# Kernel optimization log

Hardware: AMD Instinct MI355X
Metric: run time of the kernel (lower is better)

The kernel has to match this reference:

```python
import jax, jax.numpy as jnp
import numpy as np

B, T, TEMP, H, M = 2048, 168, 128, 1024, 48


def lstm_cell(x, h, c, Wih, Whh, bih, bhh):
    # PyTorch gate order: i, f, g, o
    gates = x @ Wih.T + h @ Whh.T + bih + bhh  # [B, 4H]
    i, f, g, o = jnp.split(gates, 4, axis=-1)
    i = jax.nn.sigmoid(i)
    f = jax.nn.sigmoid(f)
    g = jnp.tanh(g)
    o = jax.nn.sigmoid(o)
    c_new = f * c + i * g
    h_new = o * jnp.tanh(c_new)
    return h_new, c_new


def setup_inputs() -> dict:
    key = jax.random.key(0)
    ks = jax.random.split(key, 12)
    s_e = 1.0 / np.sqrt(H)
    u = lambda k, shape: jax.random.uniform(k, shape, jnp.float32, -s_e, s_e)
    return {
        "temp_seq": jax.random.normal(ks[0], (B, T, TEMP), jnp.float32),
        "avg_speeds": jax.random.normal(ks[1], (B, M), jnp.float32),
        "enc_Wih": u(ks[2], (4 * H, TEMP)),
        "enc_Whh": u(ks[3], (4 * H, H)),
        "enc_bih": u(ks[4], (4 * H,)),
        "enc_bhh": u(ks[5], (4 * H,)),
        "dec_Wih": u(ks[6], (4 * H, TEMP + 1)),
        "dec_Whh": u(ks[7], (4 * H, H)),
        "dec_bih": u(ks[8], (4 * H,)),
        "dec_bhh": u(ks[9], (4 * H,)),
        "fc_W": u(ks[10], (TEMP, H)),
        "fc_b": u(ks[11], (TEMP,)),
    }


def reference(temp_seq, avg_speeds, enc_Wih, enc_Whh, enc_bih, enc_bhh,
              dec_Wih, dec_Whh, dec_bih, dec_bhh, fc_W, fc_b):
    b = temp_seq.shape[0]
    h0 = jnp.zeros((b, H), temp_seq.dtype)
    c0 = jnp.zeros((b, H), temp_seq.dtype)

    # Encoder: LSTM over time, keep only final (h, c)
    def enc_step(carry, x_t):
        h, c = carry
        h, c = lstm_cell(x_t, h, c, enc_Wih, enc_Whh, enc_bih, enc_bhh)
        return (h, c), None

    (h_n, c_n), _ = jax.lax.scan(enc_step, (h0, c0), jnp.swapaxes(temp_seq, 0, 1))

    input_temp0 = temp_seq[:, -1, :]  # [B, TEMP]

    def dec_step(carry, speed_t):
        h, c, x_temp = carry
        x = jnp.concatenate([x_temp, speed_t[:, None]], axis=-1)  # [B, TEMP+1]
        h, c = lstm_cell(x, h, c, dec_Wih, dec_Whh, dec_bih, dec_bhh)
        pred = h @ fc_W.T + fc_b  # [B, TEMP]
        return (h, c, pred), pred

    _, preds = jax.lax.scan(dec_step, (h_n, c_n, input_temp0),
                            jnp.swapaxes(avg_speeds, 0, 1))
    return jnp.swapaxes(preds, 0, 1)  # [B, M, TEMP]
```

## Files before the change

### kernel.cpp

```cpp
#include <hip/hip_runtime.h>
#include <stdint.h>

#define B_SZ   2048
#define T_ENC  168
#define TEMPD  128
#define HID    1024
#define M_DEC  48

typedef _Float16 f16;
typedef _Float16 half8 __attribute__((ext_vector_type(8)));
typedef float    f32x4 __attribute__((ext_vector_type(4)));

__device__ __forceinline__ float sigf(float x)   { return 1.0f / (1.0f + __expf(-x)); }
__device__ __forceinline__ float tanhf_(float x) { return 2.0f / (1.0f + __expf(-2.0f * x)) - 1.0f; }

__device__ __forceinline__ void gld16(const void* g, void* l) {
    __builtin_amdgcn_global_load_lds(
        (const __attribute__((address_space(1))) void*)g,
        (__attribute__((address_space(3))) void*)l, 16, 0, 0);
}

__global__ void prep_xseq(const float* __restrict__ temp_seq, f16* __restrict__ xseq)
{
    size_t i4 = ((size_t)blockIdx.x * blockDim.x + threadIdx.x) * 4;
    size_t b  = i4 / (T_ENC * TEMPD);
    size_t r  = i4 - b * (T_ENC * TEMPD);
    size_t t  = r >> 7;
    size_t d  = r & 127;
    float4 v = *(const float4*)(temp_seq + i4);
    f16* o = xseq + ((t * B_SZ) + b) * TEMPD + d;
    o[0] = (f16)v.x; o[1] = (f16)v.y; o[2] = (f16)v.z; o[3] = (f16)v.w;
}

__global__ void prep_misc(
    const float* __restrict__ encWih, const float* __restrict__ encWhh,
    const float* __restrict__ decWih, const float* __restrict__ decWhh,
    const float* __restrict__ encbih, const float* __restrict__ encbhh,
    const float* __restrict__ decbih, const float* __restrict__ decbhh,
    const float* __restrict__ fcW,
    f16* __restrict__ Wenc, f16* __restrict__ Wdec0, f16* __restrict__ fcWh,
    float* __restrict__ enc_b, float* __restrict__ dec_b, float* __restrict__ wlast)
{
    const int NW = 4 * HID * (TEMPD + HID);
    for (int idx = blockIdx.x * blockDim.x + threadIdx.x; idx < NW;
         idx += gridDim.x * blockDim.x) {
        int j = idx / (TEMPD + HID);
        int k = idx - j * (TEMPD + HID);
        Wenc[idx]  = (f16)(k < TEMPD ? encWih[j * TEMPD + k]
                                     : encWhh[(size_t)j * HID + (k - TEMPD)]);
        Wdec0[idx] = (f16)(k < TEMPD ? decWih[j * (TEMPD + 1) + k]
                                     : decWhh[(size_t)j * HID + (k - TEMPD)]);
        if (idx < TEMPD * HID) fcWh[idx] = (f16)fcW[idx];
        if (idx < 4 * HID) {
            enc_b[idx] = encbih[idx] + encbhh[idx];
            dec_b[idx] = decbih[idx] + decbhh[idx];
            wlast[idx] = decWih[idx * (TEMPD + 1) + TEMPD];
        }
    }
}

__global__ __launch_bounds__(256)
void prep_fold(
    const float* __restrict__ decWih, const float* __restrict__ decWhh,
    const float* __restrict__ decbih, const float* __restrict__ decbhh,
    const float* __restrict__ fcW,    const float* __restrict__ fcb,
    f16* __restrict__ WdecF, float* __restrict__ biasF)
{
    __shared__ float wih[16][TEMPD];
    __shared__ float fcbL[TEMPD];
    const int tid = threadIdx.x;
    const int j0  = blockIdx.x * 16;
    for (int i = tid; i < 16 * TEMPD; i += 256) {
        int r = i >> 7, p = i & 127;
        wih[r][p] = decWih[(size_t)(j0 + r) * (TEMPD + 1) + p];
    }
    if (tid < TEMPD) fcbL[tid] = fcb[tid];
    __syncthreads();
    for (int kk = 0; kk < 4; ++kk) {
        int k = kk * 256 + tid;
        float acc[16];
        #pragma unroll
        for (int r = 0; r < 16; ++r) acc[r] = decWhh[(size_t)(j0 + r) * HID + k];
        for (int p = 0; p < TEMPD; ++p) {
            float w = fcW[(size_t)p * HID + k];
            #pragma unroll
            for (int r = 0; r < 16; ++r) acc[r] += wih[r][p] * w;
        }
        #pragma unroll
        for (int r = 0; r < 16; ++r) WdecF[(size_t)(j0 + r) * HID + k] = (f16)acc[r];
    }
    if (tid < 16) {
        float b = decbih[j0 + tid] + decbhh[j0 + tid];
        for (int p = 0; p < TEMPD; ++p) b += wih[tid][p] * fcbL[p];
        biasF[j0 + tid] = b;
    }
}

__global__ void prep_tileW(const f16* __restrict__ Wsrc, f16* __restrict__ Wt,
                           int NKC, int WS)
{
    int idx = blockIdx.x * blockDim.x + threadIdx.x;
    int total = 32 * NKC * 16 * 64;
    if (idx >= total) return;
    int lane = idx & 63;
    int f    = idx >> 6;
    int wc   = f & 1;
    int g    = (f >> 1) & 3;
    int s    = (f >> 3) & 1;
    int kc   = (f >> 4) % NKC;
    int bn   = (f >> 4) / NKC;
    int row  = g * HID + bn * 32 + wc * 16 + (lane & 15);
    int k0   = kc * 64 + s * 32 + (lane >> 4) * 8;
    *(half8*)(Wt + (size_t)idx * 8) = *(const half8*)(Wsrc + (size_t)row * WS + k0);
}

template <int FULLK, int DEC>
__global__ __launch_bounds__(256, 2)
void lstm_step(
    const f16* __restrict__ xsrc,
    const f16* __restrict__ h_in, f16* __restrict__ h_out, float* __restrict__ c,
    const f16* __restrict__ Wt,
    const float* __restrict__ bias,
    const float* __restrict__ wlast, const float* __restrict__ speeds, int m_step)
{
    constexpr int NKC = FULLK ? 18 : 16;

    __shared__ half8 ldsA[2][1024];

    const int tid  = threadIdx.x;
    const int lane = tid & 63;
    const int wid  = tid >> 6;
    const int wr   = wid >> 1;
    const int wc   = wid & 1;
    const int id   = blockIdx.x;
    const int swzb = (id & 7) * 64 + (id >> 3);
    const int bn   = swzb >> 4;
    const int bm   = swzb & 15;

    const half8* wtb = (const half8*)Wt + ((size_t)bn * NKC * 16) * 64 + wc * 64 + lane;

    f32x4 acc[4][4];
    #pragma unroll
    for (int g = 0; g < 4; ++g)
        #pragma unroll
        for (int mr = 0; mr < 4; ++mr)
            acc[g][mr] = (f32x4){0.f, 0.f, 0.f, 0.f};

    auto stageA = [&](int b, int kc) {
        if (FULLK && kc < 2) {
            #pragma unroll
            for (int it = 0; it < 4; ++it) {
                int p = wid * 256 + it * 64 + lane;
                int row = p >> 3, s = p & 7;
                gld16(xsrc + (size_t)(bm * 128 + row) * TEMPD + kc * 64 + ((s ^ (row & 7)) << 3),
                      &ldsA[b][wid * 256 + it * 64]);
            }
        } else {
            const int k0 = kc * 64 - (FULLK ? TEMPD : 0);
            #pragma unroll
            for (int it = 0; it < 4; ++it) {
                int p = wid * 256 + it * 64 + lane;
                int row = p >> 3, s = p & 7;
                gld16(h_in + (size_t)(bm * 128 + row) * HID + k0 + ((s ^ (row & 7)) << 3),
                      &ldsA[b][wid * 256 + it * 64]);
            }
        }
    };
    auto loadW = [&](half8 (&wf)[8], int kc) {
        const half8* p = wtb + (size_t)kc * (16 * 64);
        #pragma unroll
        for (int f = 0; f < 8; ++f) wf[f] = p[f * 128];
    };
    auto compute = [&](int b, const half8 (&wf)[8]) {
        #pragma unroll
        for (int s = 0; s < 2; ++s) {
            const int ks = s * 4 + (lane >> 4);
            half8 af[4];
            #pragma unroll
            for (int mr = 0; mr < 4; ++mr) {
                int row = wr * 64 + mr * 16 + (lane & 15);
                af[mr] = ldsA[b][row * 8 + (ks ^ (row & 7))];
            }
            __builtin_amdgcn_s_setprio(1);
            #pragma unroll
            for (int g = 0; g < 4; ++g)
                #pragma unroll
                for (int mr = 0; mr < 4; ++mr)
                    acc[g][mr] = __builtin_amdgcn_mfma_f32_16x16x32_f16(af[mr], wf[s * 4 + g], acc[g][mr], 0, 0, 0);
            __builtin_amdgcn_s_setprio(0);
        }
    };

    half8 wfA[8], wfB[8];
    stageA(0, 0); loadW(wfA, 0);
    __syncthreads();

    for (int kc = 0; kc < NKC; kc += 2) {
        stageA(1, kc + 1); loadW(wfB, kc + 1);
        compute(0, wfA);
        __syncthreads();
        if (kc + 2 < NKC) { stageA(0, kc + 2); loadW(wfA, kc + 2); }
        compute(1, wfB);
        __syncthreads();
    }

    const int col_g = bn * 32 + wc * 16 + (lane & 15);
    const float bi  = bias[col_g];
    const float bf_ = bias[HID + col_g];
    const float bg  = bias[2 * HID + col_g];
    const float bo  = bias[3 * HID + col_g];
    float wli = 0.f, wlf = 0.f, wlg = 0.f, wlo = 0.f;
    if (DEC) {
        wli = wlast[col_g];
        wlf = wlast[HID + col_g];
        wlg = wlast[2 * HID + col_g];
        wlo = wlast[3 * HID + col_g];
    }
    #pragma unroll
    for (int mr = 0; mr < 4; ++mr) {
        #pragma unroll
        for (int q = 0; q < 4; ++q) {
            int row_g = bm * 128 + wr * 64 + mr * 16 + (lane >> 4) * 4 + q;
            float pi = acc[0][mr][q] + bi;
            float pf = acc[1][mr][q] + bf_;
            float pg = acc[2][mr][q] + bg;
            float po = acc[3][mr][q] + bo;
            if (DEC) {
                float sp = speeds[(size_t)row_g * M_DEC + m_step];
                pi += sp * wli; pf += sp * wlf; pg += sp * wlg; po += sp * wlo;
            }
            float ii = sigf(pi), ff = sigf(pf), gg = tanhf_(pg), oo = sigf(po);
            size_t idx = (size_t)row_g * HID + col_g;
            float cn = ff * c[idx] + ii * gg;
            c[idx] = cn;
            h_out[idx] = (f16)(oo * tanhf_(cn));
        }
    }
}

__global__ __launch_bounds__(256, 2)
void fc_batch(const f16* __restrict__ hist, const f16* __restrict__ fcWh,
              const float* __restrict__ fcb, float* __restrict__ out, int mbase)
{
    __shared__ half8 ldsA[32 * 8];
    __shared__ half8 ldsW[128 * 8];
    const int tid  = threadIdx.x;
    const int lane = tid & 63;
    const int wid  = tid >> 6;
    const int wr   = wid >> 1;
    const int wc   = wid & 1;
    const int bm   = blockIdx.x;
    const int slot = bm >> 6;
    const int b0   = (bm & 63) * 32;
    const f16* hrow = hist + (size_t)slot * (B_SZ * HID) + (size_t)b0 * HID;
    const int  mm   = mbase + slot;

    f32x4 acc[4];
    #pragma unroll
    for (int nr = 0; nr < 4; ++nr) acc[nr] = (f32x4){0.f, 0.f, 0.f, 0.f};

    for (int kc = 0; kc < HID / 64; ++kc) {
        const int k0 = kc * 64;
        {
            int row = tid >> 3, s = tid & 7;
            gld16(hrow + (size_t)row * HID + k0 + ((s ^ (row & 7)) << 3), &ldsA[wid * 64]);
        }
        #pragma unroll
        for (int it = 0; it < 4; ++it) {
            int p = wid * 256 + it * 64 + lane;
            int row = p >> 3, s = p & 7;
            gld16(fcWh + (size_t)row * HID + k0 + ((s ^ (row & 7)) << 3), &ldsW[wid * 256 + it * 64]);
        }
        __syncthreads();
        #pragma unroll
        for (int s2 = 0; s2 < 2; ++s2) {
            int arow = wr * 16 + (lane & 15);
            int slotk = s2 * 4 + (lane >> 4);
            half8 a = ldsA[arow * 8 + (slotk ^ (arow & 7))];
            #pragma unroll
            for (int nr = 0; nr < 4; ++nr) {
                int brow = wc * 64 + nr * 16 + (lane & 15);
                half8 bfr = ldsW[brow * 8 + (slotk ^ (brow & 7))];
                acc[nr] = __builtin_amdgcn_mfma_f32_16x16x32_f16(a, bfr, acc[nr], 0, 0, 0);
            }
        }
        __syncthreads();
    }
    #pragma unroll
    for (int nr = 0; nr < 4; ++nr)
        #pragma unroll
        for (int q = 0; q < 4; ++q) {
            int rloc = wr * 16 + (lane >> 4) * 4 + q;
            int col  = wc * 64 + nr * 16 + (lane & 15);
            out[(size_t)(b0 + rloc) * (M_DEC * TEMPD) + (size_t)mm * TEMPD + col] = acc[nr][q] + fcb[col];
        }
}

extern "C" void kernel_launch(void* const* d_in, const int* in_sizes, int n_in,
                              void* d_out, int out_size, void* d_ws, size_t ws_size,
                              hipStream_t stream)
{
    (void)in_sizes; (void)n_in; (void)out_size; (void)ws_size;
    const float* temp_seq   = (const float*)d_in[0];
    const float* avg_speeds = (const float*)d_in[1];
    const float* enc_Wih    = (const float*)d_in[2];
    const float* enc_Whh    = (const float*)d_in[3];
    const float* enc_bih    = (const float*)d_in[4];
    const float* enc_bhh    = (const float*)d_in[5];
    const float* dec_Wih    = (const float*)d_in[6];
    const float* dec_Whh    = (const float*)d_in[7];
    const float* dec_bih    = (const float*)d_in[8];
    const float* dec_bhh    = (const float*)d_in[9];
    const float* fc_W       = (const float*)d_in[10];
    const float* fc_b       = (const float*)d_in[11];
    float* out = (float*)d_out;

    char* ws = (char*)d_ws;
    size_t off = 0;
    auto alloc = [&](size_t bytes) -> void* {
        void* p = ws + off;
        off += (bytes + 255) & ~(size_t)255;
        return p;
    };
    const size_t SLOT = (size_t)B_SZ * HID;
    f16*   Wenc   = (f16*)alloc((size_t)4 * HID * (TEMPD + HID) * 2);
    f16*   Wdec0  = (f16*)alloc((size_t)4 * HID * (TEMPD + HID) * 2);
    f16*   WdecF  = (f16*)alloc((size_t)4 * HID * HID * 2);
    f16*   WencT  = (f16*)alloc((size_t)32 * 18 * 16 * 64 * 8 * 2);
    f16*   Wdec0T = (f16*)alloc((size_t)32 * 18 * 16 * 64 * 8 * 2);
    f16*   WdecFT = (f16*)alloc((size_t)32 * 16 * 16 * 64 * 8 * 2);
    f16*   fcWh   = (f16*)alloc((size_t)TEMPD * HID * 2);
    float* enc_b  = (float*)alloc((size_t)4 * HID * 4);
    float* dec_b  = (float*)alloc((size_t)4 * HID * 4);
    float* biasF  = (float*)alloc((size_t)4 * HID * 4);
    float* wlast  = (float*)alloc((size_t)4 * HID * 4);
    f16*   hA     = (f16*)alloc(SLOT * 2);
    f16*   hB     = (f16*)alloc(SLOT * 2);
    float* cbuf   = (float*)alloc(SLOT * 4);
    f16*   xseq   = (f16*)alloc((size_t)T_ENC * B_SZ * TEMPD * 2);
    f16*   hist   = (f16*)alloc(16 * SLOT * 2);

    hipMemsetAsync(hA,   0, SLOT * 2, stream);
    hipMemsetAsync(cbuf, 0, SLOT * 4, stream);

    prep_xseq<<<(B_SZ * T_ENC * TEMPD / 4 + 255) / 256, 256, 0, stream>>>(temp_seq, xseq);
    prep_misc<<<8192, 256, 0, stream>>>(
        enc_Wih, enc_Whh, dec_Wih, dec_Whh,
        enc_bih, enc_bhh, dec_bih, dec_bhh, fc_W,
        Wenc, Wdec0, fcWh, enc_b, dec_b, wlast);
    prep_fold<<<256, 256, 0, stream>>>(
        dec_Wih, dec_Whh, dec_bih, dec_bhh, fc_W, fc_b, WdecF, biasF);
    prep_tileW<<<(32 * 18 * 16 * 64 + 255) / 256, 256, 0, stream>>>(Wenc,  WencT,  18, TEMPD + HID);
    prep_tileW<<<(32 * 18 * 16 * 64 + 255) / 256, 256, 0, stream>>>(Wdec0, Wdec0T, 18, TEMPD + HID);
    prep_tileW<<<(32 * 16 * 16 * 64 + 255) / 256, 256, 0, stream>>>(WdecF, WdecFT, 16, HID);

    f16* hbuf[2] = {hA, hB};
    for (int t = 0; t < T_ENC; ++t) {
        lstm_step<1, 0><<<512, 256, 0, stream>>>(
            xseq + (size_t)t * (B_SZ * TEMPD),
            hbuf[t & 1], hbuf[(t + 1) & 1], cbuf,
            WencT, enc_b, nullptr, nullptr, 0);
    }
    for (int m = 0; m < M_DEC; ++m) {
        const f16* hin = (m == 0) ? hA : hist + ((size_t)((m - 1) & 15)) * SLOT;
        f16* hout = hist + ((size_t)(m & 15)) * SLOT;
        if (m == 0) {
            lstm_step<1, 1><<<512, 256, 0, stream>>>(
                xseq + (size_t)(T_ENC - 1) * (B_SZ * TEMPD),
                hin, hout, cbuf, Wdec0T, dec_b, wlast, avg_speeds, 0);
        } else {
            lstm_step<0, 1><<<512, 256, 0, stream>>>(
                nullptr, hin, hout, cbuf, WdecFT, biasF, wlast, avg_speeds, m);
        }
        if ((m & 15) == 15) {
            fc_batch<<<1024, 256, 0, stream>>>(hist, fcWh, fc_b, out, m - 15);
        }
    }
}
```

Measured before the change: 6.319 ms.

## Fuse all LSTM steps into one persistent kernel with a software grid barrier

Replaces the 216 per-step kernel launches and the three FC batch launches with a single persistent kernel of 512 blocks. Blocks step through the encoder and decoder timesteps and synchronise with an atomic generation-counter grid barrier between steps. The FC projection over all 48 stored decoder states then runs at the end, so the history buffer grows to 48 slots. This is meant to remove launch and drain gaps between steps, but correctness depends on all 512 blocks being co-resident. The barrier also has a spin timeout that could break synchronisation silently.

New measurement: 18.04 ms. 186% more time.

```diff
diff --git a/kernel.cpp b/kernel.cpp
--- a/kernel.cpp
+++ b/kernel.cpp
@@ -6,6 +6,7 @@
 #define TEMPD  128
 #define HID    1024
 #define M_DEC  48
+#define NBLK   512
 
 typedef _Float16 f16;
 typedef _Float16 half8 __attribute__((ext_vector_type(8)));
@@ -114,19 +115,43 @@
     *(half8*)(Wt + (size_t)idx * 8) = *(const half8*)(Wsrc + (size_t)row * WS + k0);
 }
 
-template <int FULLK, int DEC>
+struct PK {
+    const f16* xseq; f16* hA; f16* hB; float* c;
+    const f16* WencT; const f16* Wdec0T; const f16* WdecFT;
+    const float* enc_b; const float* dec_b; const float* biasF;
+    const float* wlast; const float* speeds;
+    f16* hist; const f16* fcWh; const float* fcb; float* out;
+    unsigned* cnt; unsigned* gen;
+};
+
+__device__ __forceinline__ void gridbar(unsigned* cnt, unsigned* gen)
+{
+    __syncthreads();
+    if (threadIdx.x == 0) {
+        unsigned g = __hip_atomic_load(gen, __ATOMIC_RELAXED, __HIP_MEMORY_SCOPE_AGENT);
+        __builtin_amdgcn_fence(__ATOMIC_RELEASE, "agent");
+        unsigned a = __hip_atomic_fetch_add(cnt, 1u, __ATOMIC_RELAXED, __HIP_MEMORY_SCOPE_AGENT);
+        if (a == NBLK - 1) {
+            __hip_atomic_store(cnt, 0u, __ATOMIC_RELAXED, __HIP_MEMORY_SCOPE_AGENT);
+            __hip_atomic_store(gen, g + 1u, __ATOMIC_RELEASE, __HIP_MEMORY_SCOPE_AGENT);
+        } else {
+            long spin = 0;
+            while (__hip_atomic_load(gen, __ATOMIC_RELAXED, __HIP_MEMORY_SCOPE_AGENT) == g) {
+                __builtin_amdgcn_s_sleep(1);
+                if (++spin > 400000) break;
+            }
+        }
+        __builtin_amdgcn_fence(__ATOMIC_ACQUIRE, "agent");
+    }
+    __syncthreads();
+}
+
 __global__ __launch_bounds__(256, 2)
-void lstm_step(
-    const f16* __restrict__ xsrc,
-    const f16* __restrict__ h_in, f16* __restrict__ h_out, float* __restrict__ c,
-    const f16* __restrict__ Wt,
-    const float* __restrict__ bias,
-    const float* __restrict__ wlast, const float* __restrict__ speeds, int m_step)
-{
-    constexpr int NKC = FULLK ? 18 : 16;
-
-    __shared__ half8 ldsA[2][1024];
-
+void persist(PK p)
+{
+    __shared__ half8 smem[2048];
+
+    const size_t SLOT = (size_t)B_SZ * HID;
     const int tid  = threadIdx.x;
     const int lane = tid & 63;
     const int wid  = tid >> 6;
@@ -137,163 +162,176 @@
     const int bn   = swzb >> 4;
     const int bm   = swzb & 15;
 
-    const half8* wtb = (const half8*)Wt + ((size_t)bn * NKC * 16) * 64 + wc * 64 + lane;
-
-    f32x4 acc[4][4];
-    #pragma unroll
-    for (int g = 0; g < 4; ++g)
-        #pragma unroll
-        for (int mr = 0; mr < 4; ++mr)
-            acc[g][mr] = (f32x4){0.f, 0.f, 0.f, 0.f};
-
-    auto stageA = [&](int b, int kc) {
-        if (FULLK && kc < 2) {
+    for (int step = 0; step < T_ENC + M_DEC; ++step) {
+        const int m = step - T_ENC;
+        const f16* Wt; const float* bias; const f16* xsrc;
+        const f16* hin; f16* hout;
+        int nkc, fullk, dec;
+        if (step < T_ENC) {
+            Wt = p.WencT; bias = p.enc_b; nkc = 18; fullk = 1; dec = 0;
+            xsrc = p.xseq + (size_t)step * (B_SZ * TEMPD);
+            hin  = (step & 1) ? p.hB : p.hA;
+            hout = (step & 1) ? p.hA : p.hB;
+        } else if (m == 0) {
+            Wt = p.Wdec0T; bias = p.dec_b; nkc = 18; fullk = 1; dec = 1;
+            xsrc = p.xseq + (size_t)(T_ENC - 1) * (B_SZ * TEMPD);
+            hin  = p.hA;
+            hout = p.hist;
+        } else {
+            Wt = p.WdecFT; bias = p.biasF; nkc = 16; fullk = 0; dec = 1;
+            xsrc = nullptr;
+            hin  = p.hist + (size_t)(m - 1) * SLOT;
+            hout = p.hist + (size_t)m * SLOT;
+        }
+        const half8* wtb = (const half8*)Wt + (size_t)bn * nkc * 16 * 64 + wc * 64 + lane;
+
+        f32x4 acc[4][4];
+        #pragma unroll
+        for (int g = 0; g < 4; ++g)
+            #pragma unroll
+            for (int mr = 0; mr < 4; ++mr)
+                acc[g][mr] = (f32x4){0.f, 0.f, 0.f, 0.f};
+
+        auto stageA = [&](int b, int kc) {
+            if (fullk && kc < 2) {
+                #pragma unroll
+                for (int it = 0; it < 4; ++it) {
+                    int pc = wid * 256 + it * 64 + lane;
+                    int row = pc >> 3, s = pc & 7;
+                    gld16(xsrc + (size_t)(bm * 128 + row) * TEMPD + kc * 64 + ((s ^ (row & 7)) << 3),
+                          &smem[b * 1024 + wid * 256 + it * 64]);
+                }
+            } else {
+                const int k0 = kc * 64 - (fullk ? TEMPD : 0);
+                #pragma unroll
+                for (int it = 0; it < 4; ++it) {
+                    int pc = wid * 256 + it * 64 + lane;
+                    int row = pc >> 3, s = pc & 7;
+                    gld16(hin + (size_t)(bm * 128 + row) * HID + k0 + ((s ^ (row & 7)) << 3),
+                          &smem[b * 1024 + wid * 256 + it * 64]);
+                }
+            }
+        };
+        auto loadW = [&](half8 (&wf)[8], int kc) {
+            const half8* pw = wtb + (size_t)kc * (16 * 64);
+            #pragma unroll
+            for (int f = 0; f < 8; ++f) wf[f] = pw[f * 128];
+        };
+        auto compute = [&](int b, const half8 (&wf)[8]) {
+            #pragma unroll
+            for (int s = 0; s < 2; ++s) {
+                const int ks = s * 4 + (lane >> 4);
+                half8 af[4];
+                #pragma unroll
+                for (int mr = 0; mr < 4; ++mr) {
+                    int row = wr * 64 + mr * 16 + (lane & 15);
+                    af[mr] = smem[b * 1024 + row * 8 + (ks ^ (row & 7))];
+                }
+                __builtin_amdgcn_s_setprio(1);
+                #pragma unroll
+                for (int g = 0; g < 4; ++g)
+                    #pragma unroll
+                    for (int mr = 0; mr < 4; ++mr)
+                        acc[g][mr] = __builtin_amdgcn_mfma_f32_16x16x32_f16(af[mr], wf[s * 4 + g], acc[g][mr], 0, 0, 0);
+                __builtin_amdgcn_s_setprio(0);
+            }
+        };
+
+        half8 wfA[8], wfB[8];
+        stageA(0, 0); loadW(wfA, 0);
+        __syncthreads();
+        for (int kc = 0; kc < nkc; kc += 2) {
+            stageA(1, kc + 1); loadW(wfB, kc + 1);
+            compute(0, wfA);
+            __syncthreads();
+            if (kc + 2 < nkc) { stageA(0, kc + 2); loadW(wfA, kc + 2); }
+            compute(1, wfB);
+            __syncthreads();
+        }
+
+        const int col_g = bn * 32 + wc * 16 + (lane & 15);
+        const float bi  = bias[col_g];
+        const float bf_ = bias[HID + col_g];
+        const float bg  = bias[2 * HID + col_g];
+        const float bo  = bias[3 * HID + col_g];
+        float wli = 0.f, wlf = 0.f, wlg = 0.f, wlo = 0.f;
+        if (dec) {
+            wli = p.wlast[col_g];
+            wlf = p.wlast[HID + col_g];
+            wlg = p.wlast[2 * HID + col_g];
+            wlo = p.wlast[3 * HID + col_g];
+        }
+        #pragma unroll
+        for (int mr = 0; mr < 4; ++mr) {
+            #pragma unroll
+            for (int q = 0; q < 4; ++q) {
+                int row_g = bm * 128 + wr * 64 + mr * 16 + (lane >> 4) * 4 + q;
+                float pi = acc[0][mr][q] + bi;
+                float pf = acc[1][mr][q] + bf_;
+                float pg = acc[2][mr][q] + bg;
+                float po = acc[3][mr][q] + bo;
+                if (dec) {
+                    float sp = p.speeds[(size_t)row_g * M_DEC + m];
+                    pi += sp * wli; pf += sp * wlf; pg += sp * wlg; po += sp * wlo;
+                }
+                float ii = sigf(pi), ff = sigf(pf), gg = tanhf_(pg), oo = sigf(po);
+                size_t idx = (size_t)row_g * HID + col_g;
+                float cn = ff * p.c[idx] + ii * gg;
+                p.c[idx] = cn;
+                hout[idx] = (f16)(oo * tanhf_(cn));
+            }
+        }
+
+        gridbar(p.cnt, p.gen);
+    }
+
+    for (int tile = id; tile < M_DEC * 64; tile += NBLK) {
+        const int slot = tile >> 6;
+        const int b0   = (tile & 63) * 32;
+        const f16* hrow = p.hist + (size_t)slot * SLOT + (size_t)b0 * HID;
+
+        f32x4 facc[4];
+        #pragma unroll
+        for (int nr = 0; nr < 4; ++nr) facc[nr] = (f32x4){0.f, 0.f, 0.f, 0.f};
+
+        for (int kc = 0; kc < HID / 64; ++kc) {
+            const int k0 = kc * 64;
+            {
+                int row = tid >> 3, s = tid & 7;
+                gld16(hrow + (size_t)row * HID + k0 + ((s ^ (row & 7)) << 3), &smem[wid * 64]);
+            }
             #pragma unroll
             for (int it = 0; it < 4; ++it) {
-                int p = wid * 256 + it * 64 + lane;
-                int row = p >> 3, s = p & 7;
-                gld16(xsrc + (size_t)(bm * 128 + row) * TEMPD + kc * 64 + ((s ^ (row & 7)) << 3),
-                      &ldsA[b][wid * 256 + it * 64]);
-            }
-        } else {
-            const int k0 = kc * 64 - (FULLK ? TEMPD : 0);
-            #pragma unroll
-            for (int it = 0; it < 4; ++it) {
-                int p = wid * 256 + it * 64 + lane;
-                int row = p >> 3, s = p & 7;
-                gld16(h_in + (size_t)(bm * 128 + row) * HID + k0 + ((s ^ (row & 7)) << 3),
-                      &ldsA[b][wid * 256 + it * 64]);
-            }
-        }
-    };
-    auto loadW = [&](half8 (&wf)[8], int kc) {
-        const half8* p = wtb + (size_t)kc * (16 * 64);
-        #pragma unroll
-        for (int f = 0; f < 8; ++f) wf[f] = p[f * 128];
-    };
-    auto compute = [&](int b, const half8 (&wf)[8]) {
-        #pragma unroll
-        for (int s = 0; s < 2; ++s) {
-            const int ks = s * 4 + (lane >> 4);
-            half8 af[4];
-            #pragma unroll
-            for (int mr = 0; mr < 4; ++mr) {
-                int row = wr * 64 + mr * 16 + (lane & 15);
-                af[mr] = ldsA[b][row * 8 + (ks ^ (row & 7))];
-            }
-            __builtin_amdgcn_s_setprio(1);
-            #pragma unroll
-            for (int g = 0; g < 4; ++g)
+                int pc = wid * 256 + it * 64 + lane;
+                int row = pc >> 3, s = pc & 7;
+                gld16(p.fcWh + (size_t)row * HID + k0 + ((s ^ (row & 7)) << 3),
+                      &smem[256 + wid * 256 + it * 64]);
+            }
+            __syncthreads();
+            #pragma unroll
+            for (int s2 = 0; s2 < 2; ++s2) {
+                int arow = wr * 16 + (lane & 15);
+                int ks = s2 * 4 + (lane >> 4);
+                half8 a = smem[arow * 8 + (ks ^ (arow & 7))];
                 #pragma unroll
-                for (int mr = 0; mr < 4; ++mr)
-                    acc[g][mr] = __builtin_amdgcn_mfma_f32_16x16x32_f16(af[mr], wf[s * 4 + g], acc[g][mr], 0, 0, 0);
-            __builtin_amdgcn_s_setprio(0);
-        }
-    };
-
-    half8 wfA[8], wfB[8];
-    stageA(0, 0); loadW(wfA, 0);
-    __syncthreads();
-
-    for (int kc = 0; kc < NKC; kc += 2) {
-        stageA(1, kc + 1); loadW(wfB, kc + 1);
-        compute(0, wfA);
-        __syncthreads();
-        if (kc + 2 < NKC) { stageA(0, kc + 2); loadW(wfA, kc + 2); }
-        compute(1, wfB);
-        __syncthreads();
-    }
-
-    const int col_g = bn * 32 + wc * 16 + (lane & 15);
-    const float bi  = bias[col_g];
-    const float bf_ = bias[HID + col_g];
-    const float bg  = bias[2 * HID + col_g];
-    const float bo  = bias[3 * HID + col_g];
-    float wli = 0.f, wlf = 0.f, wlg = 0.f, wlo = 0.f;
-    if (DEC) {
-        wli = wlast[col_g];
-        wlf = wlast[HID + col_g];
-        wlg = wlast[2 * HID + col_g];
-        wlo = wlast[3 * HID + col_g];
-    }
-    #pragma unroll
-    for (int mr = 0; mr < 4; ++mr) {
-        #pragma unroll
-        for (int q = 0; q < 4; ++q) {
-            int row_g = bm * 128 + wr * 64 + mr * 16 + (lane >> 4) * 4 + q;
-            float pi = acc[0][mr][q] + bi;
-            float pf = acc[1][mr][q] + bf_;
-            float pg = acc[2][mr][q] + bg;
-            float po = acc[3][mr][q] + bo;
-            if (DEC) {
-                float sp = speeds[(size_t)row_g * M_DEC + m_step];
-                pi += sp * wli; pf += sp * wlf; pg += sp * wlg; po += sp * wlo;
-            }
-            float ii = sigf(pi), ff = sigf(pf), gg = tanhf_(pg), oo = sigf(po);
-            size_t idx = (size_t)row_g * HID + col_g;
-            float cn = ff * c[idx] + ii * gg;
-            c[idx] = cn;
-            h_out[idx] = (f16)(oo * tanhf_(cn));
-        }
-    }
-}
-
-__global__ __launch_bounds__(256, 2)
-void fc_batch(const f16* __restrict__ hist, const f16* __restrict__ fcWh,
-              const float* __restrict__ fcb, float* __restrict__ out, int mbase)
-{
-    __shared__ half8 ldsA[32 * 8];
-    __shared__ half8 ldsW[128 * 8];
-    const int tid  = threadIdx.x;
-    const int lane = tid & 63;
-    const int wid  = tid >> 6;
-    const int wr   = wid >> 1;
-    const int wc   = wid & 1;
-    const int bm   = blockIdx.x;
-    const int slot = bm >> 6;
-    const int b0   = (bm & 63) * 32;
-    const f16* hrow = hist + (size_t)slot * (B_SZ * HID) + (size_t)b0 * HID;
-    const int  mm   = mbase + slot;
-
-    f32x4 acc[4];
-    #pragma unroll
-    for (int nr = 0; nr < 4; ++nr) acc[nr] = (f32x4){0.f, 0.f, 0.f, 0.f};
-
-    for (int kc = 0; kc < HID / 64; ++kc) {
-        const int k0 = kc * 64;
-        {
-            int row = tid >> 3, s = tid & 7;
-            gld16(hrow + (size_t)row * HID + k0 + ((s ^ (row & 7)) << 3), &ldsA[wid * 64]);
-        }
-        #pragma unroll
-        for (int it = 0; it < 4; ++it) {
-            int p = wid * 256 + it * 64 + lane;
-            int row = p >> 3, s = p & 7;
-            gld16(fcWh + (size_t)row * HID + k0 + ((s ^ (row & 7)) << 3), &ldsW[wid * 256 + it * 64]);
-        }
-        __syncthreads();
-        #pragma unroll
-        for (int s2 = 0; s2 < 2; ++s2) {
-            int arow = wr * 16 + (lane & 15);
-            int slotk = s2 * 4 + (lane >> 4);
-            half8 a = ldsA[arow * 8 + (slotk ^ (arow & 7))];
-            #pragma unroll
-            for (int nr = 0; nr < 4; ++nr) {
-                int brow = wc * 64 + nr * 16 + (lane & 15);
-                half8 bfr = ldsW[brow * 8 + (slotk ^ (brow & 7))];
-                acc[nr] = __builtin_amdgcn_mfma_f32_16x16x32_f16(a, bfr, acc[nr], 0, 0, 0);
-            }
-        }
-        __syncthreads();
-    }
-    #pragma unroll
-    for (int nr = 0; nr < 4; ++nr)
-        #pragma unroll
-        for (int q = 0; q < 4; ++q) {
-            int rloc = wr * 16 + (lane >> 4) * 4 + q;
-            int col  = wc * 64 + nr * 16 + (lane & 15);
-            out[(size_t)(b0 + rloc) * (M_DEC * TEMPD) + (size_t)mm * TEMPD + col] = acc[nr][q] + fcb[col];
-        }
+                for (int nr = 0; nr < 4; ++nr) {
+                    int brow = wc * 64 + nr * 16 + (lane & 15);
+                    half8 bfr = smem[256 + brow * 8 + (ks ^ (brow & 7))];
+                    facc[nr] = __builtin_amdgcn_mfma_f32_16x16x32_f16(a, bfr, facc[nr], 0, 0, 0);
+                }
+            }
+            __syncthreads();
+        }
+        #pragma unroll
+        for (int nr = 0; nr < 4; ++nr)
+            #pragma unroll
+            for (int q = 0; q < 4; ++q) {
+                int rloc = wr * 16 + (lane >> 4) * 4 + q;
+                int col  = wc * 64 + nr * 16 + (lane & 15);
+                p.out[(size_t)(b0 + rloc) * (M_DEC * TEMPD) + (size_t)slot * TEMPD + col]
+                    = facc[nr][q] + p.fcb[col];
+            }
+    }
 }
 
 extern "C" void kernel_launch(void* const* d_in, const int* in_sizes, int n_in,
@@ -338,10 +376,12 @@
     f16*   hB     = (f16*)alloc(SLOT * 2);
     float* cbuf   = (float*)alloc(SLOT * 4);
     f16*   xseq   = (f16*)alloc((size_t)T_ENC * B_SZ * TEMPD * 2);
-    f16*   hist   = (f16*)alloc(16 * SLOT * 2);
+    f16*   hist   = (f16*)alloc((size_t)M_DEC * SLOT * 2);
+    unsigned* bar = (unsigned*)alloc(256);
 
     hipMemsetAsync(hA,   0, SLOT * 2, stream);
     hipMemsetAsync(cbuf, 0, SLOT * 4, stream);
+    hipMemsetAsync(bar,  0, 256, stream);
 
     prep_xseq<<<(B_SZ * T_ENC * TEMPD / 4 + 255) / 256, 256, 0, stream>>>(temp_seq, xseq);
     prep_misc<<<8192, 256, 0, stream>>>(
@@ -354,26 +394,13 @@
     prep_tileW<<<(32 * 18 * 16 * 64 + 255) / 256, 256, 0, stream>>>(Wdec0, Wdec0T, 18, TEMPD + HID);
     prep_tileW<<<(32 * 16 * 16 * 64 + 255) / 256, 256, 0, stream>>>(WdecF, WdecFT, 16, HID);
 
-    f16* hbuf[2] = {hA, hB};
-    for (int t = 0; t < T_ENC; ++t) {
-        lstm_step<1, 0><<<512, 256, 0, stream>>>(
-            xseq + (size_t)t * (B_SZ * TEMPD),
-            hbuf[t & 1], hbuf[(t + 1) & 1], cbuf,
-            WencT, enc_b, nullptr, nullptr, 0);
-    }
-    for (int m = 0; m < M_DEC; ++m) {
-        const f16* hin = (m == 0) ? hA : hist + ((size_t)((m - 1) & 15)) * SLOT;
-        f16* hout = hist + ((size_t)(m & 15)) * SLOT;
-        if (m == 0) {
-            lstm_step<1, 1><<<512, 256, 0, stream>>>(
-                xseq + (size_t)(T_ENC - 1) * (B_SZ * TEMPD),
-                hin, hout, cbuf, Wdec0T, dec_b, wlast, avg_speeds, 0);
-        } else {
-            lstm_step<0, 1><<<512, 256, 0, stream>>>(
-                nullptr, hin, hout, cbuf, WdecFT, biasF, wlast, avg_speeds, m);
-        }
-        if ((m & 15) == 15) {
-            fc_batch<<<1024, 256, 0, stream>>>(hist, fcWh, fc_b, out, m - 15);
-        }
-    }
-}
+    PK pk;
+    pk.xseq = xseq; pk.hA = hA; pk.hB = hB; pk.c = cbuf;
+    pk.WencT = WencT; pk.Wdec0T = Wdec0T; pk.WdecFT = WdecFT;
+    pk.enc_b = enc_b; pk.dec_b = dec_b; pk.biasF = biasF;
+    pk.wlast = wlast; pk.speeds = avg_speeds;
+    pk.hist = hist; pk.fcWh = fcWh; pk.fcb = fc_b; pk.out = out;
+    pk.cnt = bar; pk.gen = bar + 1;
+
+    persist<<<dim3(NBLK), dim3(256), 0, stream>>>(pk);
+}
```
